# Kernel tuning notes

Hardware: AMD Instinct MI355X
Metric: run time of the kernel (lower is better)

## Reference

```python
import jax, jax.numpy as jnp
from jax import lax
import numpy as np

N, C, H, W = 8, 32, 64, 64
KS, NB = 7, 6            # kernel_size, num_bases
TB = (KS // 2) * NB      # total_bases = 18
BC = TB * NB             # bc_dim = 108
INTER = max(64, BC // 2) # 64
OUT = 64
PAD = KS // 2
EPS = 1e-5


def conv3x3(x, w, b):
    # x: (N,Cin,H,W), w: (Cout,Cin,3,3)
    y = lax.conv_general_dilated(x, w, (1, 1), [(1, 1), (1, 1)],
                                 dimension_numbers=('NCHW', 'OIHW', 'NCHW'))
    return y + b[None, :, None, None]


def batchnorm(x, g, b):
    # training-mode BN: batch stats over (N,H,W)
    mu = jnp.mean(x, axis=(0, 2, 3), keepdims=True)
    var = jnp.var(x, axis=(0, 2, 3), keepdims=True)
    return (x - mu) * lax.rsqrt(var + EPS) * g[None, :, None, None] + b[None, :, None, None]


def setup_inputs() -> dict:
    key = jax.random.key(0)
    ks = jax.random.split(key, 12)
    s = 0.05
    # random bases as in get_random_bases: (TB, KS*KS), zero-mean-ish rows
    f = jax.random.normal(ks[0], (TB, KS * KS), dtype=jnp.float32)
    bases = f - jnp.mean(f, axis=1, keepdims=True) / jnp.std(f, axis=1, keepdims=True)
    return {
        'x': jax.random.normal(ks[1], (N, C, H, W), dtype=jnp.float32),
        'conv1_w': jax.random.normal(ks[2], (INTER, C, 3, 3), dtype=jnp.float32) * s,
        'conv1_b': jax.random.normal(ks[3], (INTER,), dtype=jnp.float32) * s,
        'bn1_g': jnp.ones((INTER,), jnp.float32),
        'bn1_b': jnp.zeros((INTER,), jnp.float32),
        'conv2_w': jax.random.normal(ks[4], (BC, INTER, 3, 3), dtype=jnp.float32) * s,
        'conv2_b': jax.random.normal(ks[5], (BC,), dtype=jnp.float32) * s,
        'bn2_g': jnp.ones((BC,), jnp.float32),
        'bn2_b': jnp.zeros((BC,), jnp.float32),
        'bases': bases,
        'out_w': jax.random.normal(ks[6], (OUT, C * NB), dtype=jnp.float32) * s,
        'out_b': jax.random.normal(ks[7], (OUT,), dtype=jnp.float32) * s,
    }


def reference(x, conv1_w, conv1_b, bn1_g, bn1_b, conv2_w, conv2_b,
              bn2_g, bn2_b, bases, out_w, out_b):
    # bases_net: conv3x3 -> BN -> tanh -> conv3x3 -> BN -> tanh
    h = jnp.tanh(batchnorm(conv3x3(x, conv1_w, conv1_b), bn1_g, bn1_b))
    coef = jnp.tanh(batchnorm(conv3x3(h, conv2_w, conv2_b), bn2_g, bn2_b))
    # (N, BC, H, W) -> (N, NB, TB, H, W) -> (N, H, W, NB, TB)
    coef = coef.reshape(N, NB, TB, H, W).transpose(0, 3, 4, 1, 2)
    # atoms: (coef[...,None] * bases).sum(-2).transpose(-1,-2) => (N,H,W,KS^2,NB)
    atoms = jnp.einsum('nhwmt,tk->nhwkm', coef, bases)
    # unfold: channel-major (C, ks, ks) flattened, matching F.unfold
    patches = lax.conv_general_dilated_patches(
        x, (KS, KS), (1, 1), [(PAD, PAD), (PAD, PAD)],
        dimension_numbers=('NCHW', 'OIHW', 'NCHW'))  # (N, C*KS*KS, H, W)
    patches = patches.reshape(N, C, KS * KS, H, W)
    # per-pixel contraction over ks^2: (N,H,W,C,NB)
    bases_out = jnp.einsum('nckhw,nhwkm->nhwcm', patches, atoms)
    bases_out = bases_out.reshape(N, H, W, C * NB)
    out = jnp.einsum('nhwd,od->nohw', bases_out, out_w) + out_b[None, :, None, None]
    return out
```

## Files before the change

### kernel.cpp

```cpp
#include <hip/hip_runtime.h>
#include <hip/hip_bf16.h>

#define N_ 8
#define C_ 32
#define H_ 64
#define W_ 64
#define HW_ (H_*W_)
#define NHW_ (N_*HW_)
#define INTER_ 64
#define BC_ 108
#define KS_ 7
#define K2_ (KS_*KS_)
#define NB_ 6
#define TB_ 18
#define OUT_ 64
#define DDIM_ (C_*NB_)
#define P2CH_ 288

typedef __attribute__((ext_vector_type(8))) short short8;
typedef __attribute__((ext_vector_type(4))) float f32x4;

__device__ __forceinline__ unsigned short f2bf(float f) {
    union { float f; unsigned u; } v; v.f = f;
    unsigned r = v.u + 0x7fffu + ((v.u >> 16) & 1u);
    return (unsigned short)(r >> 16);
}
__device__ __forceinline__ float bf2f(unsigned short h) {
    return __uint_as_float((unsigned int)h << 16);
}

__device__ __forceinline__ short8 frag4(const unsigned int* p) {
    union { unsigned int u[4]; short8 s; } v;
    v.u[0] = p[0]; v.u[1] = p[1]; v.u[2] = p[2]; v.u[3] = p[3];
    return v.s;
}

__inline__ __device__ float wave_reduce_sum(float v) {
    #pragma unroll
    for (int off = 32; off > 0; off >>= 1) v += __shfl_down(v, off);
    return v;
}

__global__ __launch_bounds__(256) void k_prep(const float* __restrict__ x,
                                              const float* __restrict__ w1,
                                              const float* __restrict__ w2,
                                              const float* __restrict__ ow,
                                              unsigned short* __restrict__ xb,
                                              unsigned short* __restrict__ wb1,
                                              unsigned short* __restrict__ wb2,
                                              unsigned short* __restrict__ wbp) {
    __shared__ unsigned short sT[64 * 36];
    int bid = blockIdx.x, t = threadIdx.x;
    if (bid < 512) {
        int n = bid >> 6, hw0 = (bid << 6) & 4095;
        for (int i = t; i < 2048; i += 256) {
            int c = i >> 6, px = i & 63;
            float v = x[(((size_t)n * C_ + c) << 12) + hw0 + px];
            sT[px * 36 + c] = f2bf(v);
        }
        __syncthreads();
        unsigned int* xd = (unsigned int*)xb;
        for (int i = t; i < 1024; i += 256) {
            int px = i >> 4, cw = i & 15;
            unsigned int lo = sT[px * 36 + cw * 2], hi = sT[px * 36 + cw * 2 + 1];
            xd[(((size_t)n << 12) + hw0 + px) * 16 + cw] = lo | (hi << 16);
        }
    } else if (bid < 584) {
        int i = (bid - 512) * 256 + t;
        int ci = i & 31, co = (i >> 5) & 63, s = i >> 11;
        wb1[i] = f2bf(w1[((co << 5) + ci) * 9 + s]);
    } else if (bid < 872) {
        int i = (bid - 584) * 256 + t;
        int ci = i & 63, co = (i >> 6) & 127, s = i >> 13;
        unsigned short v = 0;
        if (co < BC_) v = f2bf(w2[((co << 6) + ci) * 9 + s]);
        wb2[i] = v;
    } else {
        int i = (bid - 872) * 256 + t;
        if (i < OUT_ * DDIM_) {
            float v = ow[i];
            unsigned short hi = f2bf(v);
            wbp[i] = hi;
            wbp[OUT_ * DDIM_ + i] = f2bf(v - bf2f(hi));
        }
    }
}

template<int CIN, int COG, int ROWS, int WPAD, int NCOQ>
__global__ __launch_bounds__(256) void k_conv3(const unsigned short* __restrict__ xb,
                                               const unsigned short* __restrict__ wb,
                                               const float* __restrict__ bias,
                                               float* __restrict__ y,
                                               int COUT_real) {
    constexpr int CPAD = CIN + 8;
    constexpr int NSLC = (ROWS + 2) * 66;
    constexpr int MT = COG / 16;
    constexpr int NTW = ROWS;
    constexpr int KSTEPS = CIN / 32;
    __shared__ unsigned short sx[NSLC * CPAD];
    __shared__ unsigned short sw[9 * COG * CPAD];

    int bid = blockIdx.x;
    int coq = bid % NCOQ;
    int rp = (bid / NCOQ) % (H_ / ROWS);
    int n = bid / (NCOQ * (H_ / ROWS));
    int h0 = rp * ROWS;
    int co0 = coq * COG;
    int t = threadIdx.x;
    int lane = t & 63, wv = t >> 6;
    int q = lane >> 4, n15 = lane & 15;

    {
        const unsigned int* xg = (const unsigned int*)xb + (size_t)n * HW_ * (CIN / 2);
        unsigned int* sxd = (unsigned int*)sx;
        constexpr int DW = CIN / 2;
        constexpr int DWPT = DW / 8;
        int part = t & 7;
        for (int sl = (t >> 3); sl < NSLC; sl += 32) {
            int r = sl / 66, col = sl % 66;
            int hh = h0 - 1 + r, ww = col - 1;
            unsigned int v[DWPT];
            #pragma unroll
            for (int i = 0; i < DWPT; i++) v[i] = 0;
            if (hh >= 0 && hh < H_ && ww >= 0 && ww < W_) {
                const unsigned int* gp = xg + (size_t)(hh * W_ + ww) * DW + part * DWPT;
                #pragma unroll
                for (int i = 0; i < DWPT; i++) v[i] = gp[i];
            }
            unsigned int* d = sxd + sl * (CPAD / 2) + part * DWPT;
            #pragma unroll
            for (int i = 0; i < DWPT; i++) d[i] = v[i];
        }
    }
    {
        const unsigned int* wg = (const unsigned int*)wb;
        unsigned int* swd = (unsigned int*)sw;
        constexpr int TOT = 9 * COG * (CIN / 2);
        for (int e = t; e < TOT; e += 256) {
            int s_co = e / (CIN / 2), cw = e % (CIN / 2);
            int s = s_co / COG, co = s_co % COG;
            swd[s_co * (CPAD / 2) + cw] = wg[((size_t)s * WPAD + co0 + co) * (CIN / 2) + cw];
        }
    }
    __syncthreads();

    f32x4 acc[NTW][MT];
    #pragma unroll
    for (int a = 0; a < NTW; a++)
        #pragma unroll
        for (int m = 0; m < MT; m++) acc[a][m] = (f32x4){0.f, 0.f, 0.f, 0.f};

    #pragma unroll
    for (int s = 0; s < 9; s++) {
        int dy = s / 3, dx = s % 3;
        #pragma unroll
        for (int kc = 0; kc < KSTEPS; kc++) {
            int ci0 = kc * 32;
            short8 bfr[NTW];
            #pragma unroll
            for (int ntl = 0; ntl < NTW; ntl++) {
                int nt = wv * NTW + ntl;
                int r_out = nt >> 2, col0 = (nt & 3) * 16;
                bfr[ntl] = *(const short8*)(sx + ((r_out + dy) * 66 + col0 + n15 + dx) * CPAD + ci0 + q * 8);
            }
            #pragma unroll
            for (int mt = 0; mt < MT; mt++) {
                short8 afr = *(const short8*)(sw + ((s * COG) + mt * 16 + n15) * CPAD + ci0 + q * 8);
                #pragma unroll
                for (int ntl = 0; ntl < NTW; ntl++)
                    acc[ntl][mt] = __builtin_amdgcn_mfma_f32_16x16x32_bf16(afr, bfr[ntl], acc[ntl][mt], 0, 0, 0);
            }
        }
    }

    #pragma unroll
    for (int ntl = 0; ntl < NTW; ntl++) {
        int nt = wv * NTW + ntl;
        int h = h0 + (nt >> 2), wcol = (nt & 3) * 16 + n15;
        #pragma unroll
        for (int mt = 0; mt < MT; mt++) {
            #pragma unroll
            for (int reg = 0; reg < 4; reg++) {
                int co = co0 + mt * 16 + q * 4 + reg;
                if (co < COUT_real)
                    y[(((size_t)n * COUT_real + co) << 12) + h * W_ + wcol] = acc[ntl][mt][reg] + bias[co];
            }
        }
    }
}

__global__ __launch_bounds__(256) void k_bnpart(const float* __restrict__ y,
                                                float2* __restrict__ part, int Cout) {
    int bid = blockIdx.x;
    int c = bid >> 3, n = bid & 7;
    int t = threadIdx.x;
    const float* p = y + (((size_t)n * Cout + c) << 12) + t * 16;
    float s = 0.f, s2 = 0.f;
    #pragma unroll
    for (int j = 0; j < 4; j++) {
        float4 v = *(const float4*)(p + j * 4);
        s += v.x + v.y + v.z + v.w;
        s2 += v.x * v.x + v.y * v.y + v.z * v.z + v.w * v.w;
    }
    s = wave_reduce_sum(s);
    s2 = wave_reduce_sum(s2);
    __shared__ float sm[8];
    int wid = t >> 6, lane = t & 63;
    if (lane == 0) { sm[wid] = s; sm[4 + wid] = s2; }
    __syncthreads();
    if (t == 0) {
        float2 r;
        r.x = sm[0] + sm[1] + sm[2] + sm[3];
        r.y = sm[4] + sm[5] + sm[6] + sm[7];
        part[c * 8 + n] = r;
    }
}

__global__ __launch_bounds__(256) void k_bntr(const float* __restrict__ y1,
                                              const float2* __restrict__ part,
                                              const float* __restrict__ g,
                                              const float* __restrict__ bb,
                                              unsigned short* __restrict__ y1b) {
    __shared__ unsigned short sT[64 * 68];
    __shared__ float scs[INTER_], shs[INTER_];
    int bid = blockIdx.x, t = threadIdx.x;
    int n = bid >> 6, hw0 = (bid << 6) & 4095;
    if (t < INTER_) {
        float s = 0.f, s2 = 0.f;
        #pragma unroll
        for (int j = 0; j < 8; j++) { float2 p = part[t * 8 + j]; s += p.x; s2 += p.y; }
        float mu = s / (float)NHW_, var = s2 / (float)NHW_ - mu * mu;
        float sc = g[t] * rsqrtf(var + 1e-5f);
        scs[t] = sc; shs[t] = bb[t] - mu * sc;
    }
    __syncthreads();
    for (int i = t; i < 4096; i += 256) {
        int c = i >> 6, px = i & 63;
        float v = y1[(((size_t)n * INTER_ + c) << 12) + hw0 + px];
        sT[px * 68 + c] = f2bf(tanhf(v * scs[c] + shs[c]));
    }
    __syncthreads();
    unsigned int* yd = (unsigned int*)y1b;
    for (int i = t; i < 2048; i += 256) {
        int px = i >> 5, cw = i & 31;
        unsigned int lo = sT[px * 68 + cw * 2], hi = sT[px * 68 + cw * 2 + 1];
        yd[(((size_t)n << 12) + hw0 + px) * 32 + cw] = lo | (hi << 16);
    }
}

__global__ __launch_bounds__(256) void k_pconv(const float* __restrict__ x,
                                               const float* __restrict__ bases,
                                               unsigned int* __restrict__ P2) {
    __shared__ float sx[70][44];
    int bid = blockIdx.x;
    int rq = bid & 3;
    int c  = (bid >> 2) & 31;
    int n  = bid >> 7;
    int t = threadIdx.x;
    int lane = t & 63, wv = t >> 6;
    int r0 = rq << 4;

    const float* xc = x + (((size_t)n * C_ + c) << 12);
    #pragma unroll
    for (int j = 0; j < 6; j++) {
        int p = wv + 4 * j;
        if (p < 22) {
            int grow = r0 - 3 + p;
            bool rowok = (grow >= 0 && grow < H_);
            int wx = lane - 3;
            float v = 0.f;
            if (rowok && wx >= 0) v = xc[(grow << 6) + wx];
            sx[lane][p] = v;
            if (lane < 6) {
                int wx2 = 61 + lane;
                float v2 = 0.f;
                if (rowok && wx2 < W_) v2 = xc[(grow << 6) + wx2];
                sx[64 + lane][p] = v2;
            }
        }
    }
    __syncthreads();

    int rb = wv * 4;
    float a0[9][4], a1[9][4];
    #pragma unroll
    for (int tp = 0; tp < 9; tp++)
        #pragma unroll
        for (int rr = 0; rr < 4; rr++) { a0[tp][rr] = 0.f; a1[tp][rr] = 0.f; }

    #pragma unroll 1
    for (int kx = 0; kx < 7; kx++) {
        float rw[12];
        const float* sp = &sx[lane + kx][rb];
        #pragma unroll
        for (int qq = 0; qq < 3; qq++) {
            float4 r4 = *(const float4*)(sp + qq * 4);
            rw[qq * 4 + 0] = r4.x; rw[qq * 4 + 1] = r4.y;
            rw[qq * 4 + 2] = r4.z; rw[qq * 4 + 3] = r4.w;
        }
        #pragma unroll
        for (int tp = 0; tp < 9; tp++) {
            #pragma unroll
            for (int ky = 0; ky < 7; ky++) {
                float w0 = bases[(2 * tp) * K2_ + ky * 7 + kx];
                float w1 = bases[(2 * tp + 1) * K2_ + ky * 7 + kx];
                #pragma unroll
                for (int rr = 0; rr < 4; rr++) {
                    float xv = rw[rr + ky];
                    a0[tp][rr] += xv * w0;
                    a1[tp][rr] += xv * w1;
                }
            }
        }
    }

    #pragma unroll
    for (int tp = 0; tp < 9; tp++)
        #pragma unroll
        for (int rr = 0; rr < 4; rr++) {
            int gr = r0 + rb + rr;
            unsigned int pk = (unsigned int)f2bf(a0[tp][rr]) | ((unsigned int)f2bf(a1[tp][rr]) << 16);
            P2[(((size_t)n * P2CH_ + tp * 32 + c) << 12) + (gr << 6) + lane] = pk;
        }
}

#define YPAD_ 97
__global__ __launch_bounds__(256) void k_ytail(const float* __restrict__ y2,
                                               const float2* __restrict__ part,
                                               const float* __restrict__ g,
                                               const float* __restrict__ bb,
                                               const unsigned int* __restrict__ P2,
                                               const unsigned short* __restrict__ wbp,
                                               const float* __restrict__ out_b,
                                               float* __restrict__ out) {
    __shared__ float scs[BC_], shs[BC_];
    __shared__ float cfs[BC_][32];
    __shared__ unsigned int sYh[32 * YPAD_];
    __shared__ unsigned int sYl[32 * YPAD_];

    int bid = blockIdx.x;
    int n = bid >> 7, px0 = (bid & 127) << 5;
    int t = threadIdx.x;

    if (t < BC_) {
        float s = 0.f, s2 = 0.f;
        #pragma unroll
        for (int j = 0; j < 8; j++) { float2 p = part[t * 8 + j]; s += p.x; s2 += p.y; }
        float mu = s / (float)NHW_, var = s2 / (float)NHW_ - mu * mu;
        float sc = g[t] * rsqrtf(var + 1e-5f);
        scs[t] = sc; shs[t] = bb[t] - mu * sc;
    }
    __syncthreads();

    for (int i = t; i < BC_ * 32; i += 256) {
        int ch = i >> 5, px = i & 31;
        float v = y2[(((size_t)n * BC_ + ch) << 12) + px0 + px];
        cfs[ch][px] = tanhf(v * scs[ch] + shs[ch]);
    }
    __syncthreads();

    {
        int px = t & 31, cg = t >> 5;
        const unsigned int* Pb = P2 + (((size_t)n * P2CH_) << 12) + px0 + px;
        unsigned int u[4][9];
        #pragma unroll
        for (int cc = 0; cc < 4; cc++) {
            int c = cg * 4 + cc;
            #pragma unroll
            for (int tp = 0; tp < 9; tp++)
                u[cc][tp] = Pb[(size_t)(tp * 32 + c) << 12];
        }
        #pragma unroll
        for (int cc = 0; cc < 4; cc++) {
            int c = cg * 4 + cc;
            float pv[TB_];
            #pragma unroll
            for (int tp = 0; tp < 9; tp++) {
                pv[2 * tp]     = __uint_as_float(u[cc][tp] << 16);
                pv[2 * tp + 1] = __uint_as_float(u[cc][tp] & 0xffff0000u);
            }
            float ym[NB_];
            #pragma unroll
            for (int m = 0; m < NB_; m++) {
                float a = 0.f;
                #pragma unroll
                for (int tt = 0; tt < TB_; tt++)
                    a += cfs[m * TB_ + tt][px] * pv[tt];
                ym[m] = a;
            }
            #pragma unroll
            for (int j = 0; j < 3; j++) {
                unsigned short h0 = f2bf(ym[2 * j]);
                unsigned short h1 = f2bf(ym[2 * j + 1]);
                unsigned short l0 = f2bf(ym[2 * j] - bf2f(h0));
                unsigned short l1 = f2bf(ym[2 * j + 1] - bf2f(h1));
                sYh[px * YPAD_ + c * 3 + j] = (unsigned int)h0 | ((unsigned int)h1 << 16);
                sYl[px * YPAD_ + c * 3 + j] = (unsigned int)l0 | ((unsigned int)l1 << 16);
            }
        }
    }
    __syncthreads();

    int lane = t & 63, wv = t >> 6;
    int q = lane >> 4, n15 = lane & 15;
    f32x4 acc[2];
    acc[0] = (f32x4){0.f, 0.f, 0.f, 0.f};
    acc[1] = (f32x4){0.f, 0.f, 0.f, 0.f};
    #pragma unroll
    for (int ks = 0; ks < 6; ks++) {
        short8 ah = *(const short8*)(wbp + (wv * 16 + n15) * DDIM_ + ks * 32 + q * 8);
        short8 al = *(const short8*)(wbp + OUT_ * DDIM_ + (wv * 16 + n15) * DDIM_ + ks * 32 + q * 8);
        #pragma unroll
        for (int nt = 0; nt < 2; nt++) {
            short8 bh = frag4(sYh + (nt * 16 + n15) * YPAD_ + ks * 16 + q * 4);
            short8 bl = frag4(sYl + (nt * 16 + n15) * YPAD_ + ks * 16 + q * 4);
            acc[nt] = __builtin_amdgcn_mfma_f32_16x16x32_bf16(ah, bh, acc[nt], 0, 0, 0);
            acc[nt] = __builtin_amdgcn_mfma_f32_16x16x32_bf16(ah, bl, acc[nt], 0, 0, 0);
            acc[nt] = __builtin_amdgcn_mfma_f32_16x16x32_bf16(al, bh, acc[nt], 0, 0, 0);
        }
    }
    #pragma unroll
    for (int nt = 0; nt < 2; nt++)
        #pragma unroll
        for (int reg = 0; reg < 4; reg++) {
            int o = wv * 16 + q * 4 + reg;
            out[(((size_t)n * OUT_ + o) << 12) + px0 + nt * 16 + n15] = acc[nt][reg] + out_b[o];
        }
}

extern "C" void kernel_launch(void* const* d_in, const int* in_sizes, int n_in,
                              void* d_out, int out_size, void* d_ws, size_t ws_size,
                              hipStream_t stream) {
    const float* x       = (const float*)d_in[0];
    const float* conv1_w = (const float*)d_in[1];
    const float* conv1_b = (const float*)d_in[2];
    const float* bn1_g   = (const float*)d_in[3];
    const float* bn1_b   = (const float*)d_in[4];
    const float* conv2_w = (const float*)d_in[5];
    const float* conv2_b = (const float*)d_in[6];
    const float* bn2_g   = (const float*)d_in[7];
    const float* bn2_b   = (const float*)d_in[8];
    const float* bases   = (const float*)d_in[9];
    const float* out_w   = (const float*)d_in[10];
    const float* out_b   = (const float*)d_in[11];
    float* out = (float*)d_out;

    float* y1  = (float*)d_ws;
    float* y2  = y1 + (size_t)N_ * INTER_ * HW_;
    unsigned int* P2 = (unsigned int*)(y2 + (size_t)N_ * BC_ * HW_);
    unsigned short* xb  = (unsigned short*)(P2 + (size_t)N_ * P2CH_ * HW_);
    unsigned short* y1b = xb + (size_t)NHW_ * C_;
    unsigned short* wb1 = y1b + (size_t)NHW_ * INTER_;
    unsigned short* wb2 = wb1 + 9 * 64 * 32;
    unsigned short* wbp = wb2 + 9 * 128 * 64;
    float2* part1 = (float2*)(wbp + 2 * OUT_ * DDIM_);
    float2* part2 = part1 + INTER_ * 8;

    k_prep<<<920, 256, 0, stream>>>(x, conv1_w, conv2_w, out_w, xb, wb1, wb2, wbp);

    k_conv3<C_, 64, 1, 64, 1><<<N_ * 64, 256, 0, stream>>>(xb, wb1, conv1_b, y1, INTER_);
    k_bnpart<<<INTER_ * 8, 256, 0, stream>>>(y1, part1, INTER_);
    k_bntr<<<512, 256, 0, stream>>>(y1, part1, bn1_g, bn1_b, y1b);

    k_conv3<INTER_, 16, 2, 128, 7><<<N_ * 32 * 7, 256, 0, stream>>>(y1b, wb2, conv2_b, y2, BC_);
    k_bnpart<<<BC_ * 8, 256, 0, stream>>>(y2, part2, BC_);

    k_pconv<<<1024, 256, 0, stream>>>(x, bases, P2);
    k_ytail<<<1024, 256, 0, stream>>>(y2, part2, bn2_g, bn2_b, P2, wbp, out_b, out);
}
```

Baseline: 204.3 us.

## Fuse BN statistics into conv epilogues and merge pconv into prep kernel

Computes the per-channel BN sum and sum-of-squares inside the conv3 epilogue with shuffle reductions and atomics, removing the two separate k_bnpart passes that re-read y1 and y2. The patch-basis convolution (k_pconv) now runs in the same launch as the weight and input conversion, along with a block that zeroes the partial-stat buffer. This cuts kernel launches and global re-reads in exchange for float atomics, which make the sums order-nondeterministic, and a larger, heterogeneous front kernel.

```diff
diff --git a/kernel.cpp b/kernel.cpp
--- a/kernel.cpp
+++ b/kernel.cpp
@@ -35,53 +35,127 @@
     return v.s;
 }
 
-__inline__ __device__ float wave_reduce_sum(float v) {
-    #pragma unroll
-    for (int off = 32; off > 0; off >>= 1) v += __shfl_down(v, off);
-    return v;
-}
-
-__global__ __launch_bounds__(256) void k_prep(const float* __restrict__ x,
-                                              const float* __restrict__ w1,
-                                              const float* __restrict__ w2,
-                                              const float* __restrict__ ow,
-                                              unsigned short* __restrict__ xb,
-                                              unsigned short* __restrict__ wb1,
-                                              unsigned short* __restrict__ wb2,
-                                              unsigned short* __restrict__ wbp) {
-    __shared__ unsigned short sT[64 * 36];
+__global__ __launch_bounds__(256) void k_front(const float* __restrict__ x,
+                                               const float* __restrict__ bases,
+                                               const float* __restrict__ w1,
+                                               const float* __restrict__ w2,
+                                               const float* __restrict__ ow,
+                                               unsigned short* __restrict__ xb,
+                                               unsigned short* __restrict__ wb1,
+                                               unsigned short* __restrict__ wb2,
+                                               unsigned short* __restrict__ wbp,
+                                               unsigned int* __restrict__ P2,
+                                               float* __restrict__ pzero) {
+    __shared__ __align__(16) char smem[70 * 44 * 4];
     int bid = blockIdx.x, t = threadIdx.x;
-    if (bid < 512) {
-        int n = bid >> 6, hw0 = (bid << 6) & 4095;
-        for (int i = t; i < 2048; i += 256) {
-            int c = i >> 6, px = i & 63;
-            float v = x[(((size_t)n * C_ + c) << 12) + hw0 + px];
-            sT[px * 36 + c] = f2bf(v);
+
+    if (bid < 1024) {
+        float (*sx)[44] = (float(*)[44])smem;
+        int rq = bid & 3;
+        int c  = (bid >> 2) & 31;
+        int n  = bid >> 7;
+        int lane = t & 63, wv = t >> 6;
+        int r0 = rq << 4;
+
+        const float* xc = x + (((size_t)n * C_ + c) << 12);
+        #pragma unroll
+        for (int j = 0; j < 6; j++) {
+            int p = wv + 4 * j;
+            if (p < 22) {
+                int grow = r0 - 3 + p;
+                bool rowok = (grow >= 0 && grow < H_);
+                int wx = lane - 3;
+                float v = 0.f;
+                if (rowok && wx >= 0) v = xc[(grow << 6) + wx];
+                sx[lane][p] = v;
+                if (lane < 6) {
+                    int wx2 = 61 + lane;
+                    float v2 = 0.f;
+                    if (rowok && wx2 < W_) v2 = xc[(grow << 6) + wx2];
+                    sx[64 + lane][p] = v2;
+                }
+            }
         }
         __syncthreads();
-        unsigned int* xd = (unsigned int*)xb;
-        for (int i = t; i < 1024; i += 256) {
-            int px = i >> 4, cw = i & 15;
-            unsigned int lo = sT[px * 36 + cw * 2], hi = sT[px * 36 + cw * 2 + 1];
-            xd[(((size_t)n << 12) + hw0 + px) * 16 + cw] = lo | (hi << 16);
-        }
-    } else if (bid < 584) {
-        int i = (bid - 512) * 256 + t;
-        int ci = i & 31, co = (i >> 5) & 63, s = i >> 11;
-        wb1[i] = f2bf(w1[((co << 5) + ci) * 9 + s]);
-    } else if (bid < 872) {
-        int i = (bid - 584) * 256 + t;
-        int ci = i & 63, co = (i >> 6) & 127, s = i >> 13;
-        unsigned short v = 0;
-        if (co < BC_) v = f2bf(w2[((co << 6) + ci) * 9 + s]);
-        wb2[i] = v;
+
+        int rb = wv * 4;
+        float a0[9][4], a1[9][4];
+        #pragma unroll
+        for (int tp = 0; tp < 9; tp++)
+            #pragma unroll
+            for (int rr = 0; rr < 4; rr++) { a0[tp][rr] = 0.f; a1[tp][rr] = 0.f; }
+
+        #pragma unroll 1
+        for (int kx = 0; kx < 7; kx++) {
+            float rw[12];
+            const float* sp = &sx[lane + kx][rb];
+            #pragma unroll
+            for (int qq = 0; qq < 3; qq++) {
+                float4 r4 = *(const float4*)(sp + qq * 4);
+                rw[qq * 4 + 0] = r4.x; rw[qq * 4 + 1] = r4.y;
+                rw[qq * 4 + 2] = r4.z; rw[qq * 4 + 3] = r4.w;
+            }
+            #pragma unroll
+            for (int tp = 0; tp < 9; tp++) {
+                #pragma unroll
+                for (int ky = 0; ky < 7; ky++) {
+                    float w0 = bases[(2 * tp) * K2_ + ky * 7 + kx];
+                    float w1v = bases[(2 * tp + 1) * K2_ + ky * 7 + kx];
+                    #pragma unroll
+                    for (int rr = 0; rr < 4; rr++) {
+                        float xv = rw[rr + ky];
+                        a0[tp][rr] += xv * w0;
+                        a1[tp][rr] += xv * w1v;
+                    }
+                }
+            }
+        }
+
+        #pragma unroll
+        for (int tp = 0; tp < 9; tp++)
+            #pragma unroll
+            for (int rr = 0; rr < 4; rr++) {
+                int gr = r0 + rb + rr;
+                unsigned int pk = (unsigned int)f2bf(a0[tp][rr]) | ((unsigned int)f2bf(a1[tp][rr]) << 16);
+                P2[(((size_t)n * P2CH_ + tp * 32 + c) << 12) + (gr << 6) + lane] = pk;
+            }
+    } else if (bid == 1944) {
+        for (int i = t; i < (INTER_ + BC_) * 8 * 2; i += 256) pzero[i] = 0.f;
     } else {
-        int i = (bid - 872) * 256 + t;
-        if (i < OUT_ * DDIM_) {
-            float v = ow[i];
-            unsigned short hi = f2bf(v);
-            wbp[i] = hi;
-            wbp[OUT_ * DDIM_ + i] = f2bf(v - bf2f(hi));
+        int pbid = bid - 1024;
+        if (pbid < 512) {
+            unsigned short* sT = (unsigned short*)smem;
+            int n = pbid >> 6, hw0 = (pbid << 6) & 4095;
+            for (int i = t; i < 2048; i += 256) {
+                int c = i >> 6, px = i & 63;
+                float v = x[(((size_t)n * C_ + c) << 12) + hw0 + px];
+                sT[px * 36 + c] = f2bf(v);
+            }
+            __syncthreads();
+            unsigned int* xd = (unsigned int*)xb;
+            for (int i = t; i < 1024; i += 256) {
+                int px = i >> 4, cw = i & 15;
+                unsigned int lo = sT[px * 36 + cw * 2], hi = sT[px * 36 + cw * 2 + 1];
+                xd[(((size_t)n << 12) + hw0 + px) * 16 + cw] = lo | (hi << 16);
+            }
+        } else if (pbid < 584) {
+            int i = (pbid - 512) * 256 + t;
+            int ci = i & 31, co = (i >> 5) & 63, s = i >> 11;
+            wb1[i] = f2bf(w1[((co << 5) + ci) * 9 + s]);
+        } else if (pbid < 872) {
+            int i = (pbid - 584) * 256 + t;
+            int ci = i & 63, co = (i >> 6) & 127, s = i >> 13;
+            unsigned short v = 0;
+            if (co < BC_) v = f2bf(w2[((co << 6) + ci) * 9 + s]);
+            wb2[i] = v;
+        } else {
+            int i = (pbid - 872) * 256 + t;
+            if (i < OUT_ * DDIM_) {
+                float v = ow[i];
+                unsigned short hi = f2bf(v);
+                wbp[i] = hi;
+                wbp[OUT_ * DDIM_ + i] = f2bf(v - bf2f(hi));
+            }
         }
     }
 }
@@ -91,6 +165,7 @@
                                                const unsigned short* __restrict__ wb,
                                                const float* __restrict__ bias,
                                                float* __restrict__ y,
+                                               float* __restrict__ part,
                                                int COUT_real) {
     constexpr int CPAD = CIN + 8;
     constexpr int NSLC = (ROWS + 2) * 66;
@@ -99,6 +174,7 @@
     constexpr int KSTEPS = CIN / 32;
     __shared__ unsigned short sx[NSLC * CPAD];
     __shared__ unsigned short sw[9 * COG * CPAD];
+    __shared__ float sbn[2][4][COG];
 
     int bid = blockIdx.x;
     int coq = bid % NCOQ;
@@ -115,7 +191,7 @@
         unsigned int* sxd = (unsigned int*)sx;
         constexpr int DW = CIN / 2;
         constexpr int DWPT = DW / 8;
-        int part = t & 7;
+        int partid = t & 7;
         for (int sl = (t >> 3); sl < NSLC; sl += 32) {
             int r = sl / 66, col = sl % 66;
             int hh = h0 - 1 + r, ww = col - 1;
@@ -123,11 +199,11 @@
             #pragma unroll
             for (int i = 0; i < DWPT; i++) v[i] = 0;
             if (hh >= 0 && hh < H_ && ww >= 0 && ww < W_) {
-                const unsigned int* gp = xg + (size_t)(hh * W_ + ww) * DW + part * DWPT;
+                const unsigned int* gp = xg + (size_t)(hh * W_ + ww) * DW + partid * DWPT;
                 #pragma unroll
                 for (int i = 0; i < DWPT; i++) v[i] = gp[i];
             }
-            unsigned int* d = sxd + sl * (CPAD / 2) + part * DWPT;
+            unsigned int* d = sxd + sl * (CPAD / 2) + partid * DWPT;
             #pragma unroll
             for (int i = 0; i < DWPT; i++) d[i] = v[i];
         }
@@ -173,6 +249,10 @@
         }
     }
 
+    float bsum[MT * 4], bsum2[MT * 4];
+    #pragma unroll
+    for (int i = 0; i < MT * 4; i++) { bsum[i] = 0.f; bsum2[i] = 0.f; }
+
     #pragma unroll
     for (int ntl = 0; ntl < NTW; ntl++) {
         int nt = wv * NTW + ntl;
@@ -182,37 +262,41 @@
             #pragma unroll
             for (int reg = 0; reg < 4; reg++) {
                 int co = co0 + mt * 16 + q * 4 + reg;
-                if (co < COUT_real)
-                    y[(((size_t)n * COUT_real + co) << 12) + h * W_ + wcol] = acc[ntl][mt][reg] + bias[co];
-            }
-        }
-    }
-}
-
-__global__ __launch_bounds__(256) void k_bnpart(const float* __restrict__ y,
-                                                float2* __restrict__ part, int Cout) {
-    int bid = blockIdx.x;
-    int c = bid >> 3, n = bid & 7;
-    int t = threadIdx.x;
-    const float* p = y + (((size_t)n * Cout + c) << 12) + t * 16;
-    float s = 0.f, s2 = 0.f;
-    #pragma unroll
-    for (int j = 0; j < 4; j++) {
-        float4 v = *(const float4*)(p + j * 4);
-        s += v.x + v.y + v.z + v.w;
-        s2 += v.x * v.x + v.y * v.y + v.z * v.z + v.w * v.w;
-    }
-    s = wave_reduce_sum(s);
-    s2 = wave_reduce_sum(s2);
-    __shared__ float sm[8];
-    int wid = t >> 6, lane = t & 63;
-    if (lane == 0) { sm[wid] = s; sm[4 + wid] = s2; }
-    __syncthreads();
-    if (t == 0) {
-        float2 r;
-        r.x = sm[0] + sm[1] + sm[2] + sm[3];
-        r.y = sm[4] + sm[5] + sm[6] + sm[7];
-        part[c * 8 + n] = r;
+                if (co < COUT_real) {
+                    float val = acc[ntl][mt][reg] + bias[co];
+                    y[(((size_t)n * COUT_real + co) << 12) + h * W_ + wcol] = val;
+                    bsum[mt * 4 + reg] += val;
+                    bsum2[mt * 4 + reg] += val * val;
+                }
+            }
+        }
+    }
+    #pragma unroll
+    for (int i = 0; i < MT * 4; i++) {
+        #pragma unroll
+        for (int mask = 1; mask < 16; mask <<= 1) {
+            bsum[i]  += __shfl_xor(bsum[i],  mask, 64);
+            bsum2[i] += __shfl_xor(bsum2[i], mask, 64);
+        }
+    }
+    if (n15 == 0) {
+        #pragma unroll
+        for (int mt = 0; mt < MT; mt++)
+            #pragma unroll
+            for (int reg = 0; reg < 4; reg++) {
+                sbn[0][wv][mt * 16 + q * 4 + reg] = bsum[mt * 4 + reg];
+                sbn[1][wv][mt * 16 + q * 4 + reg] = bsum2[mt * 4 + reg];
+            }
+    }
+    __syncthreads();
+    if (t < COG) {
+        float s = sbn[0][0][t] + sbn[0][1][t] + sbn[0][2][t] + sbn[0][3][t];
+        float s2 = sbn[1][0][t] + sbn[1][1][t] + sbn[1][2][t] + sbn[1][3][t];
+        int co = co0 + t;
+        if (co < COUT_real) {
+            atomicAdd(&part[(co * 8 + n) * 2], s);
+            atomicAdd(&part[(co * 8 + n) * 2 + 1], s2);
+        }
     }
 }
 
@@ -246,82 +330,6 @@
         unsigned int lo = sT[px * 68 + cw * 2], hi = sT[px * 68 + cw * 2 + 1];
         yd[(((size_t)n << 12) + hw0 + px) * 32 + cw] = lo | (hi << 16);
     }
-}
-
-__global__ __launch_bounds__(256) void k_pconv(const float* __restrict__ x,
-                                               const float* __restrict__ bases,
-                                               unsigned int* __restrict__ P2) {
-    __shared__ float sx[70][44];
-    int bid = blockIdx.x;
-    int rq = bid & 3;
-    int c  = (bid >> 2) & 31;
-    int n  = bid >> 7;
-    int t = threadIdx.x;
-    int lane = t & 63, wv = t >> 6;
-    int r0 = rq << 4;
-
-    const float* xc = x + (((size_t)n * C_ + c) << 12);
-    #pragma unroll
-    for (int j = 0; j < 6; j++) {
-        int p = wv + 4 * j;
-        if (p < 22) {
-            int grow = r0 - 3 + p;
-            bool rowok = (grow >= 0 && grow < H_);
-            int wx = lane - 3;
-            float v = 0.f;
-            if (rowok && wx >= 0) v = xc[(grow << 6) + wx];
-            sx[lane][p] = v;
-            if (lane < 6) {
-                int wx2 = 61 + lane;
-                float v2 = 0.f;
-                if (rowok && wx2 < W_) v2 = xc[(grow << 6) + wx2];
-                sx[64 + lane][p] = v2;
-            }
-        }
-    }
-    __syncthreads();
-
-    int rb = wv * 4;
-    float a0[9][4], a1[9][4];
-    #pragma unroll
-    for (int tp = 0; tp < 9; tp++)
-        #pragma unroll
-        for (int rr = 0; rr < 4; rr++) { a0[tp][rr] = 0.f; a1[tp][rr] = 0.f; }
-
-    #pragma unroll 1
-    for (int kx = 0; kx < 7; kx++) {
-        float rw[12];
-        const float* sp = &sx[lane + kx][rb];
-        #pragma unroll
-        for (int qq = 0; qq < 3; qq++) {
-            float4 r4 = *(const float4*)(sp + qq * 4);
-            rw[qq * 4 + 0] = r4.x; rw[qq * 4 + 1] = r4.y;
-            rw[qq * 4 + 2] = r4.z; rw[qq * 4 + 3] = r4.w;
-        }
-        #pragma unroll
-        for (int tp = 0; tp < 9; tp++) {
-            #pragma unroll
-            for (int ky = 0; ky < 7; ky++) {
-                float w0 = bases[(2 * tp) * K2_ + ky * 7 + kx];
-                float w1 = bases[(2 * tp + 1) * K2_ + ky * 7 + kx];
-                #pragma unroll
-                for (int rr = 0; rr < 4; rr++) {
-                    float xv = rw[rr + ky];
-                    a0[tp][rr] += xv * w0;
-                    a1[tp][rr] += xv * w1;
-                }
-            }
-        }
-    }
-
-    #pragma unroll
-    for (int tp = 0; tp < 9; tp++)
-        #pragma unroll
-        for (int rr = 0; rr < 4; rr++) {
-            int gr = r0 + rb + rr;
-            unsigned int pk = (unsigned int)f2bf(a0[tp][rr]) | ((unsigned int)f2bf(a1[tp][rr]) << 16);
-            P2[(((size_t)n * P2CH_ + tp * 32 + c) << 12) + (gr << 6) + lane] = pk;
-        }
 }
 
 #define YPAD_ 97
@@ -453,18 +461,19 @@
     unsigned short* wb1 = y1b + (size_t)NHW_ * INTER_;
     unsigned short* wb2 = wb1 + 9 * 64 * 32;
     unsigned short* wbp = wb2 + 9 * 128 * 64;
-    float2* part1 = (float2*)(wbp + 2 * OUT_ * DDIM_);
-    float2* part2 = part1 + INTER_ * 8;
-
-    k_prep<<<920, 256, 0, stream>>>(x, conv1_w, conv2_w, out_w, xb, wb1, wb2, wbp);
-
-    k_conv3<C_, 64, 1, 64, 1><<<N_ * 64, 256, 0, stream>>>(xb, wb1, conv1_b, y1, INTER_);
-    k_bnpart<<<INTER_ * 8, 256, 0, stream>>>(y1, part1, INTER_);
-    k_bntr<<<512, 256, 0, stream>>>(y1, part1, bn1_g, bn1_b, y1b);
-
-    k_conv3<INTER_, 16, 2, 128, 7><<<N_ * 32 * 7, 256, 0, stream>>>(y1b, wb2, conv2_b, y2, BC_);
-    k_bnpart<<<BC_ * 8, 256, 0, stream>>>(y2, part2, BC_);
-
-    k_pconv<<<1024, 256, 0, stream>>>(x, bases, P2);
-    k_ytail<<<1024, 256, 0, stream>>>(y2, part2, bn2_g, bn2_b, P2, wbp, out_b, out);
-}
+    float* part1 = (float*)(wbp + 2 * OUT_ * DDIM_);
+    float* part2 = part1 + INTER_ * 8 * 2;
+
+    k_front<<<1945, 256, 0, stream>>>(x, bases, conv1_w, conv2_w, out_w,
+                                      xb, wb1, wb2, wbp, P2, part1);
+
+    k_conv3<C_, 64, 1, 64, 1><<<N_ * 64, 256, 0, stream>>>(
+        xb, wb1, conv1_b, y1, part1, INTER_);
+    k_bntr<<<512, 256, 0, stream>>>(y1, (const float2*)part1, bn1_g, bn1_b, y1b);
+
+    k_conv3<INTER_, 16, 2, 128, 7><<<N_ * 32 * 7, 256, 0, stream>>>(
+        y1b, wb2, conv2_b, y2, part2, BC_);
+
+    k_ytail<<<1024, 256, 0, stream>>>(y2, (const float2*)part2, bn2_g, bn2_b,
+                                      P2, wbp, out_b, out);
+}
```

After: 228.6 us. 11.9% more time.
